# Kernel tuning notes

Hardware: AMD Instinct MI355X
Metric: run time of the kernel (lower is better)

Reference implementation:

```python
import jax, jax.numpy as jnp
import numpy as np

N = 4096      # num_nodes
DIN = 16      # num_inputs
C = 16        # comm_channels
CHQ = 8       # ch_q
K = 10        # value-iteration steps
GAMMA = 0.99
EPS = float(np.finfo(np.float32).eps)


def setup_inputs() -> dict:
    key = jax.random.key(0)
    ks = jax.random.split(key, 8)
    x = jax.random.normal(ks[0], (N, DIN), dtype=jnp.float32)
    comms = jnp.zeros((N, C), dtype=jnp.float32)  # fresh comm state (reset())
    # random symmetric 0/1 adjacency, ~20 avg degree, zero diagonal
    u = jax.random.uniform(ks[1], (N, N), dtype=jnp.float32)
    a = (u < 0.005).astype(jnp.float32)
    adj = jnp.maximum(a, a.T) * (1.0 - jnp.eye(N, dtype=jnp.float32))
    mask = jnp.ones((N,), dtype=jnp.float32)
    # parameters (torch Linear: y = x @ W + b, weights stored [in, out] here)
    Wr = jax.random.normal(ks[2], (DIN + C, 1), dtype=jnp.float32) * 0.1   # reward_encoding
    br = jnp.zeros((1,), dtype=jnp.float32)
    We = jax.random.normal(ks[3], (DIN + C, CHQ), dtype=jnp.float32) * 0.1  # encoder
    be = jnp.zeros((CHQ,), dtype=jnp.float32)
    w_emb = jax.random.normal(ks[4], (CHQ,), dtype=jnp.float32) * 0.1       # embedder (ch_q -> 1)
    b_emb = jnp.zeros((), dtype=jnp.float32)
    Wa = jax.random.normal(ks[5], (CHQ,), dtype=jnp.float32) * 0.1          # action_decoding (1 -> ch_q)
    ba = jnp.zeros((CHQ,), dtype=jnp.float32)
    return dict(x=x, comms=comms, adj=adj, mask=mask, Wr=Wr, br=br,
                We=We, be=be, w_emb=w_emb, b_emb=b_emb, Wa=Wa, ba=ba, k=K)


def reference(x, comms, adj, mask, Wr, br, We, be, w_emb, b_emb, Wa, ba, k):
    n = adj.shape[0]
    # initialize_adj: symmetric normalization D^{-1/2} (A + I) D^{-1/2}
    a_norm = adj + jnp.eye(n, dtype=adj.dtype)
    deg = a_norm.sum(axis=0)
    dinv_sqrt = jnp.sqrt(1.0 / (deg + EPS))
    k3 = a_norm * dinv_sqrt[:, None] * dinv_sqrt[None, :]

    xc = jnp.concatenate([x, comms], axis=1)          # [n, DIN+C]
    r = (xc @ Wr + br)[:, 0]                          # reward per node [n]
    # embedder(cols - rows) fused: score[i,j] = s[j] - s[i] + b_emb
    s = (xc @ We + be) @ w_emb                        # [n]
    kernel3 = k3 * (s[None, :] - s[:, None] + b_emb)  # [n, n]

    # k-step value iteration
    v = jnp.zeros_like(r)
    for _ in range(k):
        k3v = kernel3 @ (r + GAMMA * v)               # [n]
        q = k3v[:, None] * Wa[None, :] + ba           # action_decoding (1 -> ch_q): [n, ch_q]
        v = q.max(axis=-1)                            # [n]

    # final_feature_process (rl=False): additive -inf mask
    return v + jnp.where(mask == 0, -jnp.inf, 0.0)
```

## Files before the change

kernel.cpp:

```cpp
#include <hip/hip_runtime.h>
#include <math.h>

#define NN     4096
#define NB     256
#define TPB    1024
#define WPB    16
#define CAP    128
#define SLOT   80
#define NB2    32
#define NPB2   128
#define MAXE   10
#define GAMMA  0.99f
#define EPSF   1.1920929e-07f
#define KSTEPS 10
#define RELSTR 16


__device__ __forceinline__ unsigned long long pk2(float lo, float hi) {
    return ((unsigned long long)__float_as_uint(hi) << 32) |
            (unsigned long long)__float_as_uint(lo);
}
__device__ __forceinline__ float lo_f(unsigned long long z) {
    return __uint_as_float((unsigned int)z);
}
__device__ __forceinline__ float hi_f(unsigned long long z) {
    return __uint_as_float((unsigned int)(z >> 32));
}

__global__ void __launch_bounds__(TPB) gvin_hop1(
    const float* __restrict__ adj,  const float* __restrict__ x,
    const float* __restrict__ comms,const float* __restrict__ mask,
    const float* __restrict__ Wr,   const float* __restrict__ br,
    const float* __restrict__ We,   const float* __restrict__ be,
    const float* __restrict__ w_emb,const float* __restrict__ b_emb,
    const float* __restrict__ Wa,   const float* __restrict__ ba,
    int* arr, int* rel, int* FL,
    unsigned long long* PD, unsigned long long* RS,
    float* UF0, float* UF1, int* CNT, int* CSRG,
    float* __restrict__ out)
{
    __shared__ int nbr[WPB][CAP];
    __shared__ int lcnt[WPB];
    __shared__ unsigned long long PDL[NN];
    __shared__ float UL[NN];
    const int tid  = (int)threadIdx.x;
    const int wave = tid >> 6;
    const int lane = tid & 63;
    const int g = (int)blockIdx.x * WPB + wave;

    if (lane == 0) { lcnt[wave] = 1; nbr[wave][0] = g; }

    const float4* rowp = (const float4*)(adj + (size_t)g * NN);
#pragma unroll 4
    for (int it = 0; it < 16; ++it) {
        const float4 v = rowp[lane + it * 64];
        const int b4 = (lane + it * 64) * 4;
        if (v.x != 0.0f) { int sl = atomicAdd(&lcnt[wave], 1); if (sl < CAP) nbr[wave][sl] = b4;     }
        if (v.y != 0.0f) { int sl = atomicAdd(&lcnt[wave], 1); if (sl < CAP) nbr[wave][sl] = b4 + 1; }
        if (v.z != 0.0f) { int sl = atomicAdd(&lcnt[wave], 1); if (sl < CAP) nbr[wave][sl] = b4 + 2; }
        if (v.w != 0.0f) { int sl = atomicAdd(&lcnt[wave], 1); if (sl < CAP) nbr[wave][sl] = b4 + 3; }
    }

    float pr = 0.0f, ps = 0.0f;
    if (lane < 32) {
        const float xc = (lane < 16) ? x[g * 16 + lane] : comms[g * 16 + (lane - 16)];
        float we = 0.0f;
#pragma unroll
        for (int c = 0; c < 8; ++c) we += We[lane * 8 + c] * w_emb[c];
        pr = xc * Wr[lane];
        ps = xc * we;
    } else if (lane == 32) {
#pragma unroll
        for (int c = 0; c < 8; ++c) ps += be[c] * w_emb[c];
        pr = br[0];
    }
#pragma unroll
    for (int off = 32; off; off >>= 1) { pr += __shfl_xor(pr, off); ps += __shfl_xor(ps, off); }
    const float r = pr, s = ps;

    const int   deg  = lcnt[wave];
    const int   cl   = deg < CAP ? deg : CAP;
    const int   clp  = cl < SLOT ? cl : SLOT;
    const float dinv = sqrtf(1.0f / ((float)deg + EPSF));
    const float p    = dinv * (s + b_emb[0]);

    if (lane == 0) {
        __hip_atomic_store(PD  + g, pk2(p, dinv), __ATOMIC_RELAXED, __HIP_MEMORY_SCOPE_AGENT);
        __hip_atomic_store(RS  + g, pk2(r, s),    __ATOMIC_RELAXED, __HIP_MEMORY_SCOPE_AGENT);
        __hip_atomic_store(UF0 + g, r,            __ATOMIC_RELAXED, __HIP_MEMORY_SCOPE_AGENT);
        __hip_atomic_store(CNT + g, clp,          __ATOMIC_RELAXED, __HIP_MEMORY_SCOPE_AGENT);
    }
    if (lane < clp)
        __hip_atomic_store(CSRG + g * SLOT + lane, nbr[wave][lane],
                           __ATOMIC_RELAXED, __HIP_MEMORY_SCOPE_AGENT);
    if (64 + lane < clp)
        __hip_atomic_store(CSRG + g * SLOT + 64 + lane, nbr[wave][64 + lane],
                           __ATOMIC_RELAXED, __HIP_MEMORY_SCOPE_AGENT);

    __syncthreads();
    if (tid == 0)
        __hip_atomic_store(arr + blockIdx.x, 1, __ATOMIC_RELAXED, __HIP_MEMORY_SCOPE_AGENT);
    if (blockIdx.x >= NB2) return;
    if (blockIdx.x == 0) {
        if (tid < 64) {
            const int base = tid * 4;
            for (;;) {
                const int a0 = __hip_atomic_load(arr + base + 0, __ATOMIC_RELAXED, __HIP_MEMORY_SCOPE_AGENT);
                const int a1 = __hip_atomic_load(arr + base + 1, __ATOMIC_RELAXED, __HIP_MEMORY_SCOPE_AGENT);
                const int a2 = __hip_atomic_load(arr + base + 2, __ATOMIC_RELAXED, __HIP_MEMORY_SCOPE_AGENT);
                const int a3 = __hip_atomic_load(arr + base + 3, __ATOMIC_RELAXED, __HIP_MEMORY_SCOPE_AGENT);
                if (__all((a0 >= 1) && (a1 >= 1) && (a2 >= 1) && (a3 >= 1))) break;
                __builtin_amdgcn_s_sleep(1);
            }
            if (tid < NB2)
                __hip_atomic_store(rel + (size_t)tid * RELSTR, 1,
                                   __ATOMIC_RELAXED, __HIP_MEMORY_SCOPE_AGENT);
        }
    } else if (tid == 0) {
        while (__hip_atomic_load(rel + (size_t)blockIdx.x * RELSTR,
                                 __ATOMIC_RELAXED, __HIP_MEMORY_SCOPE_AGENT) < 1)
            __builtin_amdgcn_s_sleep(1);
    }
    __syncthreads();

    {
        unsigned long long w0, w1, w2, w3;
        asm volatile(
            "global_load_dwordx2 %0, %4, off sc1\n\t"
            "global_load_dwordx2 %1, %5, off sc1\n\t"
            "global_load_dwordx2 %2, %6, off sc1\n\t"
            "global_load_dwordx2 %3, %7, off sc1\n\t"
            "s_waitcnt vmcnt(0)"
            : "=&v"(w0), "=&v"(w1), "=&v"(w2), "=&v"(w3)
            : "v"(PD + tid), "v"(PD + tid + 1024),
              "v"(PD + tid + 2048), "v"(PD + tid + 3072)
            : "memory");
        PDL[tid] = w0; PDL[tid + 1024] = w1;
        PDL[tid + 2048] = w2; PDL[tid + 3072] = w3;
    }
    __syncthreads();

    const int q   = tid >> 3, sub = tid & 7;
    const int n   = (int)blockIdx.x * NPB2 + q;
    const int dgn = __hip_atomic_load(CNT + n, __ATOMIC_RELAXED, __HIP_MEMORY_SCOPE_AGENT);
    int jj[MAXE]; float pe[MAXE], de[MAXE];
#pragma unroll
    for (int e = 0; e < MAXE; ++e) {
        const int k  = sub + (e << 3);
        const bool vv = k < dgn;
        const int idx = n * SLOT + (vv ? k : 0);
        const int j   = __hip_atomic_load(CSRG + idx, __ATOMIC_RELAXED, __HIP_MEMORY_SCOPE_AGENT);
        jj[e] = vv ? j : 0;
        const unsigned long long z = PDL[jj[e]];
        pe[e] = vv ? lo_f(z) : 0.0f;
        de[e] = vv ? hi_f(z) : 0.0f;
    }
    float rn = 0.0f, sn = 0.0f, dvn = 0.0f;
    if (sub == 0) {
        const unsigned long long z = __hip_atomic_load(RS + n, __ATOMIC_RELAXED, __HIP_MEMORY_SCOPE_AGENT);
        rn = lo_f(z); sn = hi_f(z); dvn = hi_f(PDL[n]);
    }
    float wa[8], bb[8];
#pragma unroll
    for (int c = 0; c < 8; ++c) { wa[c] = Wa[c]; bb[c] = ba[c]; }

    float v = 0.0f;
    for (int t = 0; t < KSTEPS; ++t) {
        const float* Uf = (t & 1) ? UF1 : UF0;
        float*       Uo = (t & 1) ? UF0 : UF1;

        if (t > 0) {
            if (wave == 0 && lane < NB2) {
                while (__hip_atomic_load(
                           FL + ((size_t)blockIdx.x * NB2 + lane) * RELSTR,
                           __ATOMIC_RELAXED, __HIP_MEMORY_SCOPE_AGENT) < t)
                    __builtin_amdgcn_s_sleep(1);
            }
            __syncthreads();
        }

        {
            float f0, f1, f2, f3;
            asm volatile(
                "global_load_dword %0, %4, off sc1\n\t"
                "global_load_dword %1, %5, off sc1\n\t"
                "global_load_dword %2, %6, off sc1\n\t"
                "global_load_dword %3, %7, off sc1\n\t"
                "s_waitcnt vmcnt(0)"
                : "=&v"(f0), "=&v"(f1), "=&v"(f2), "=&v"(f3)
                : "v"(Uf + tid), "v"(Uf + tid + 1024),
                  "v"(Uf + tid + 2048), "v"(Uf + tid + 3072)
                : "memory");
            UL[tid] = f0; UL[tid + 1024] = f1;
            UL[tid + 2048] = f2; UL[tid + 3072] = f3;
        }
        __syncthreads();

        float a1 = 0.0f, a2 = 0.0f;
#pragma unroll
        for (int e = 0; e < MAXE; ++e) {
            const float u = UL[jj[e]];
            a1 = fmaf(pe[e], u, a1);
            a2 = fmaf(de[e], u, a2);
        }
        a1 += __shfl_xor(a1, 1); a2 += __shfl_xor(a2, 1);
        a1 += __shfl_xor(a1, 2); a2 += __shfl_xor(a2, 2);
        a1 += __shfl_xor(a1, 4); a2 += __shfl_xor(a2, 4);

        if (sub == 0) {
            const float k3v = dvn * (a1 - sn * a2);
            v = fmaf(k3v, wa[0], bb[0]);
#pragma unroll
            for (int c = 1; c < 8; ++c) v = fmaxf(v, fmaf(k3v, wa[c], bb[c]));
            if (t < KSTEPS - 1)
                __hip_atomic_store(Uo + n, rn + GAMMA * v,
                                   __ATOMIC_RELAXED, __HIP_MEMORY_SCOPE_AGENT);
        }
        if (t < KSTEPS - 1) {
            __syncthreads();
            if (tid < NB2)
                __hip_atomic_store(
                    FL + ((size_t)tid * NB2 + blockIdx.x) * RELSTR, t + 1,
                    __ATOMIC_RELAXED, __HIP_MEMORY_SCOPE_AGENT);
        }
    }

    if (sub == 0) out[n] = v + (mask[n] == 0.0f ? -INFINITY : 0.0f);
}

extern "C" void kernel_launch(void* const* d_in, const int* in_sizes, int n_in,
                              void* d_out, int out_size, void* d_ws, size_t ws_size,
                              hipStream_t stream) {
    const float* x     = (const float*)d_in[0];
    const float* comms = (const float*)d_in[1];
    const float* adj   = (const float*)d_in[2];
    const float* mask  = (const float*)d_in[3];
    const float* Wr    = (const float*)d_in[4];
    const float* br    = (const float*)d_in[5];
    const float* We    = (const float*)d_in[6];
    const float* be    = (const float*)d_in[7];
    const float* w_emb = (const float*)d_in[8];
    const float* b_emb = (const float*)d_in[9];
    const float* Wa    = (const float*)d_in[10];
    const float* ba    = (const float*)d_in[11];

    char* ws = (char*)d_ws;
    size_t off = 0;
    int* arr               = (int*)(ws + off); off += 4096;
    int* rel               = (int*)(ws + off); off += 4096;
    int* FL                = (int*)(ws + off); off += (size_t)NB2 * NB2 * 64;
    unsigned long long* PD = (unsigned long long*)(ws + off); off += (size_t)NN * 8;
    unsigned long long* RS = (unsigned long long*)(ws + off); off += (size_t)NN * 8;
    float* UF0             = (float*)(ws + off); off += (size_t)NN * 4;
    float* UF1             = (float*)(ws + off); off += (size_t)NN * 4;
    int* CNT               = (int*)(ws + off); off += (size_t)NN * 4;
    int* CSRG              = (int*)(ws + off); off += (size_t)NN * SLOT * 4;
    float* out = (float*)d_out;

    gvin_hop1<<<dim3(NB), dim3(TPB), 0, stream>>>(
        adj, x, comms, mask, Wr, br, We, be, w_emb, b_emb, Wa, ba,
        arr, rel, FL, PD, RS, UF0, UF1, CNT, CSRG, out);
}
```

Baseline: 147.9 us.

## Replace per-block barrier flags with per-wave flags and vectorized slice loads

Each wave now publishes its own readiness flag to every consumer block as soon as its stores have drained, instead of the whole block barrier-syncing before one flag write. On the consumer side, each wave polls only the 32 producer-wave flags covering its 256-element slice of the value vector. It then loads that slice with a single dwordx4 load, which removes the block-wide barrier between polling and loading. This is meant to shorten the per-iteration grid-wide synchronization latency, at the cost of a 16x larger flag array and more polling traffic.

```diff
diff --git a/kernel.cpp b/kernel.cpp
--- a/kernel.cpp
+++ b/kernel.cpp
@@ -16,6 +16,8 @@
 #define RELSTR 16
 
 
+typedef float f32x4 __attribute__((ext_vector_type(4)));
+
 __device__ __forceinline__ unsigned long long pk2(float lo, float hi) {
     return ((unsigned long long)__float_as_uint(hi) << 32) |
             (unsigned long long)__float_as_uint(lo);
@@ -27,14 +29,14 @@
     return __uint_as_float((unsigned int)(z >> 32));
 }
 
-__global__ void __launch_bounds__(TPB) gvin_hop1(
+__global__ void __launch_bounds__(TPB) gvin_wflag(
     const float* __restrict__ adj,  const float* __restrict__ x,
     const float* __restrict__ comms,const float* __restrict__ mask,
     const float* __restrict__ Wr,   const float* __restrict__ br,
     const float* __restrict__ We,   const float* __restrict__ be,
     const float* __restrict__ w_emb,const float* __restrict__ b_emb,
     const float* __restrict__ Wa,   const float* __restrict__ ba,
-    int* arr, int* rel, int* FL,
+    int* arr, int* rel, int* FLW,
     unsigned long long* PD, unsigned long long* RS,
     float* UF0, float* UF1, int* CNT, int* CSRG,
     float* __restrict__ out)
@@ -170,29 +172,25 @@
         float*       Uo = (t & 1) ? UF0 : UF1;
 
         if (t > 0) {
-            if (wave == 0 && lane < NB2) {
-                while (__hip_atomic_load(
-                           FL + ((size_t)blockIdx.x * NB2 + lane) * RELSTR,
-                           __ATOMIC_RELAXED, __HIP_MEMORY_SCOPE_AGENT) < t)
-                    __builtin_amdgcn_s_sleep(1);
+            const int pprod = 2 * wave + (lane >> 4 & 1);
+            const size_t fline =
+                ((size_t)blockIdx.x * (NB2 * 16) + pprod * 16 + (lane & 15)) * RELSTR;
+            for (;;) {
+                int f = t;
+                if (lane < 32)
+                    f = __hip_atomic_load(FLW + fline, __ATOMIC_RELAXED, __HIP_MEMORY_SCOPE_AGENT);
+                if (__all(f >= t)) break;
+                __builtin_amdgcn_s_sleep(1);
             }
-            __syncthreads();
-        }
-
+        }
         {
-            float f0, f1, f2, f3;
-            asm volatile(
-                "global_load_dword %0, %4, off sc1\n\t"
-                "global_load_dword %1, %5, off sc1\n\t"
-                "global_load_dword %2, %6, off sc1\n\t"
-                "global_load_dword %3, %7, off sc1\n\t"
-                "s_waitcnt vmcnt(0)"
-                : "=&v"(f0), "=&v"(f1), "=&v"(f2), "=&v"(f3)
-                : "v"(Uf + tid), "v"(Uf + tid + 1024),
-                  "v"(Uf + tid + 2048), "v"(Uf + tid + 3072)
-                : "memory");
-            UL[tid] = f0; UL[tid + 1024] = f1;
-            UL[tid + 2048] = f2; UL[tid + 3072] = f3;
+            f32x4 val;
+            asm volatile("global_load_dwordx4 %0, %1, off sc1\n\t"
+                         "s_waitcnt vmcnt(0)"
+                         : "=v"(val)
+                         : "v"(Uf + (wave << 8) + (lane << 2))
+                         : "memory");
+            *(f32x4*)&UL[(wave << 8) + (lane << 2)] = val;
         }
         __syncthreads();
 
@@ -217,11 +215,12 @@
                                    __ATOMIC_RELAXED, __HIP_MEMORY_SCOPE_AGENT);
         }
         if (t < KSTEPS - 1) {
+            asm volatile("s_waitcnt vmcnt(0)" ::: "memory");
+            if (lane < NB2)
+                __hip_atomic_store(
+                    FLW + ((size_t)lane * (NB2 * 16) + blockIdx.x * 16 + wave) * RELSTR,
+                    t + 1, __ATOMIC_RELAXED, __HIP_MEMORY_SCOPE_AGENT);
             __syncthreads();
-            if (tid < NB2)
-                __hip_atomic_store(
-                    FL + ((size_t)tid * NB2 + blockIdx.x) * RELSTR, t + 1,
-                    __ATOMIC_RELAXED, __HIP_MEMORY_SCOPE_AGENT);
         }
     }
 
@@ -248,7 +247,7 @@
     size_t off = 0;
     int* arr               = (int*)(ws + off); off += 4096;
     int* rel               = (int*)(ws + off); off += 4096;
-    int* FL                = (int*)(ws + off); off += (size_t)NB2 * NB2 * 64;
+    int* FLW               = (int*)(ws + off); off += (size_t)NB2 * NB2 * 16 * 64;
     unsigned long long* PD = (unsigned long long*)(ws + off); off += (size_t)NN * 8;
     unsigned long long* RS = (unsigned long long*)(ws + off); off += (size_t)NN * 8;
     float* UF0             = (float*)(ws + off); off += (size_t)NN * 4;
@@ -257,7 +256,7 @@
     int* CSRG              = (int*)(ws + off); off += (size_t)NN * SLOT * 4;
     float* out = (float*)d_out;
 
-    gvin_hop1<<<dim3(NB), dim3(TPB), 0, stream>>>(
+    gvin_wflag<<<dim3(NB), dim3(TPB), 0, stream>>>(
         adj, x, comms, mask, Wr, br, We, be, w_emb, b_emb, Wa, ba,
-        arr, rel, FL, PD, RS, UF0, UF1, CNT, CSRG, out);
-}
+        arr, rel, FLW, PD, RS, UF0, UF1, CNT, CSRG, out);
+}
```

After: 156.7 us. 1.06x slower.
